# Kernel tuning notes

Measured on AMD Instinct MI355X. Metric: run time of the kernel, lower is better.

Reference implementation:

```python
import jax, jax.numpy as jnp
import numpy as np

BLOCK = 16
H = 16
KV = 4
HPG = H // KV
DH = 64
SCALE = 1.0 / np.sqrt(DH).astype(np.float32)


def setup_inputs() -> dict:
    key = jax.random.key(0)
    ks = jax.random.split(key, 7)
    B, Ldec, Lenc, D = 2, 8192, 4096, 1024
    s = 1.0 / np.sqrt(D).astype(np.float32)
    return {
        "hidden_states": jax.random.normal(ks[0], (B, Ldec, D), jnp.float32),
        "encoder_hidden_states": jax.random.normal(ks[1], (B, Lenc, D), jnp.float32),
        "attention_mask": jax.random.randint(ks[2], (B, Lenc), 0, 2, jnp.int32),
        "Wq": jax.random.normal(ks[3], (D, H * DH), jnp.float32) * s,
        "Wk": jax.random.normal(ks[4], (D, KV * DH), jnp.float32) * s,
        "Wv": jax.random.normal(ks[5], (D, KV * DH), jnp.float32) * s,
        "Wo": jax.random.normal(ks[6], (H * DH, D), jnp.float32) * s,
    }


def reference(hidden_states, encoder_hidden_states, attention_mask, Wq, Wk, Wv, Wo):
    B, Ldec, D = hidden_states.shape
    Lenc = encoder_hidden_states.shape[1]
    pad = (BLOCK - Ldec % BLOCK) % BLOCK
    x = jnp.pad(hidden_states, ((0, 0), (0, pad), (0, 0))) if pad else hidden_states
    nb = (Ldec + pad) // BLOCK
    # mean-pool decoder tokens into blocks: [B, nb, D]
    pooled = x.reshape(B, nb, BLOCK, D).mean(axis=2)
    # projections; GQA: group q heads by kv head (repeat_interleave order)
    q = (pooled @ Wq).reshape(B, nb, KV, HPG, DH)          # [B, nb, KV, HPG, DH]
    k = (encoder_hidden_states @ Wk).reshape(B, Lenc, KV, DH)
    v = (encoder_hidden_states @ Wv).reshape(B, Lenc, KV, DH)
    scores = jnp.einsum("bngqd,blgd->bgqnl", q, k) * SCALE  # [B, KV, HPG, nb, Lenc]
    mask = (attention_mask == 0)[:, None, None, None, :]
    scores = jnp.where(mask, jnp.float32(-1e9), scores)
    attn = jax.nn.softmax(scores, axis=-1)
    out = jnp.einsum("bgqnl,blgd->bngqd", attn, v)          # [B, nb, KV, HPG, DH]
    out = out.reshape(B, nb, H * DH) @ Wo                   # [B, nb, D]
    # broadcast block output back to token level
    unpooled = jnp.broadcast_to(out[:, :, None, :], (B, nb, BLOCK, D)).reshape(B, nb * BLOCK, D)
    return unpooled[:, :Ldec, :]
```

## Files before the change

kernel.cpp:

```cpp
#include <hip/hip_runtime.h>


typedef unsigned short u16;
typedef __attribute__((ext_vector_type(8))) __bf16 bf16x8;
typedef __attribute__((ext_vector_type(4))) float f32x4;
typedef __attribute__((ext_vector_type(4))) _Float16 f16x4;

static __device__ __forceinline__ u16 f2bf(float f) {
    unsigned int u = __float_as_uint(f);
    u = (u + 0x7fffu + ((u >> 16) & 1u)) >> 16;
    return (u16)u;
}
static __device__ __forceinline__ void gload16(const u16* g, u16* l) {
    __builtin_amdgcn_global_load_lds(
        (const __attribute__((address_space(1))) void*)g,
        (__attribute__((address_space(3))) void*)l, 16, 0, 0);
}

__global__ __launch_bounds__(256) void prep_all(const float* __restrict__ enc,
                                                const float* __restrict__ hid,
                                                const int* __restrict__ mask,
                                                const float* __restrict__ Wq,
                                                const float* __restrict__ Wk,
                                                const float* __restrict__ Wv,
                                                const float* __restrict__ Wo,
                                                u16* __restrict__ encb,
                                                u16* __restrict__ poolb,
                                                u16* __restrict__ mh,
                                                u16* __restrict__ Wq_t,
                                                u16* __restrict__ Wkv_t,
                                                u16* __restrict__ Wo_t) {
    int bid = blockIdx.x;
    if (bid < 1024) {
        const int tid = bid * 256 + threadIdx.x;
        const int c4 = tid & 255;
        const int row = tid >> 8;
        const float4* src = (const float4*)(hid + (size_t)row * 16 * 1024) + c4;
        float4 a = src[0];
#pragma unroll
        for (int t = 1; t < 16; ++t) {
            float4 b = src[(size_t)t * 256];
            a.x += b.x; a.y += b.y; a.z += b.z; a.w += b.w;
        }
        ushort4 o;
        o.x = f2bf(a.x * 0.0625f); o.y = f2bf(a.y * 0.0625f);
        o.z = f2bf(a.z * 0.0625f); o.w = f2bf(a.w * 0.0625f);
        *(ushort4*)(poolb + (size_t)row * 1024 + c4 * 4) = o;
    } else if (bid < 3072) {
        const int base = (bid - 1024) * 1024 + threadIdx.x;
        float4 v[4];
#pragma unroll
        for (int j = 0; j < 4; ++j) v[j] = ((const float4*)enc)[base + j * 256];
#pragma unroll
        for (int j = 0; j < 4; ++j) {
            ushort4 o;
            o.x = f2bf(v[j].x); o.y = f2bf(v[j].y);
            o.z = f2bf(v[j].z); o.w = f2bf(v[j].w);
            ((ushort4*)encb)[base + j * 256] = o;
        }
    } else if (bid < 5632) {
        bid -= 3072;
        const float* in; u16* out; int N, nbx, rowoff;
        if (bid < 1024)      { in = Wq; out = Wq_t;  N = 1024; nbx = 32; rowoff = 0; }
        else if (bid < 2048) { in = Wo; out = Wo_t;  N = 1024; nbx = 32; rowoff = 0; bid -= 1024; }
        else if (bid < 2304) { in = Wk; out = Wkv_t; N = 256;  nbx = 8;  rowoff = 0; bid -= 2048; }
        else                 { in = Wv; out = Wkv_t; N = 256;  nbx = 8;  rowoff = 256; bid -= 2304; }
        const int n0 = (bid % nbx) * 32, k0 = (bid / nbx) * 32;
        __shared__ float t[32][33];
        const int tx = threadIdx.x & 31, ty = threadIdx.x >> 5;
#pragma unroll
        for (int i = 0; i < 4; ++i)
            t[ty + 8 * i][tx] = in[(size_t)(k0 + ty + 8 * i) * N + n0 + tx];
        __syncthreads();
#pragma unroll
        for (int i = 0; i < 4; ++i)
            out[(size_t)(rowoff + n0 + ty + 8 * i) * 1024 + k0 + tx] = f2bf(t[tx][ty + 8 * i]);
    } else {
#pragma unroll
        for (int k = 0; k < 32; ++k) {
            const int i = threadIdx.x + 256 * k;
            mh[i] = mask[i] ? (u16)0x3C00 : (u16)0;
        }
    }
}

template <int MODE>
static __device__ __forceinline__ void gemm_core(const u16* __restrict__ A,
                                                 const u16* __restrict__ Bt,
                                                 u16* __restrict__ outQ,
                                                 float* __restrict__ out_f,
                                                 int m0, int n0, int kt0, int nkt,
                                                 u16* sAB) {
    u16* sA = sAB;
    u16* sB = sAB + 64 * 64;
    const int t = threadIdx.x;
    const int w = t >> 6, lane = t & 63, quad = lane >> 4, r16 = lane & 15;
    const int row8 = lane >> 3, seg = lane & 7;

    f32x4 acc[4];
#pragma unroll
    for (int i = 0; i < 4; ++i) acc[i] = (f32x4){0.f, 0.f, 0.f, 0.f};

    for (int kt = kt0; kt < kt0 + nkt; ++kt) {
        const int k0 = kt * 64;
        __syncthreads();
#pragma unroll
        for (int j = 0; j < 2; ++j) {
            const int ra = w * 16 + j * 8;
            gload16(A + (size_t)(m0 + ra + row8) * 1024 + k0 + seg * 8, sA + ra * 64);
            gload16(Bt + (size_t)(n0 + ra + row8) * 1024 + k0 + seg * 8, sB + ra * 64);
        }
        __syncthreads();
#pragma unroll
        for (int kk = 0; kk < 2; ++kk) {
            const bf16x8 af = *(const bf16x8*)(sA + (16 * w + r16) * 64 + kk * 32 + quad * 8);
#pragma unroll
            for (int nt = 0; nt < 4; ++nt) {
                const bf16x8 bfv = *(const bf16x8*)(sB + (nt * 16 + r16) * 64 + kk * 32 + quad * 8);
                acc[nt] = __builtin_amdgcn_mfma_f32_16x16x32_bf16(af, bfv, acc[nt], 0, 0, 0);
            }
        }
    }

    if (MODE == 0) {
#pragma unroll
        for (int nt = 0; nt < 4; ++nt)
#pragma unroll
            for (int r = 0; r < 4; ++r) {
                const int m = m0 + 16 * w + quad * 4 + r;
                const int c = n0 + nt * 16 + r16;
                const int b = m >> 9, nq = m & 511, g = c >> 8, qh = (c >> 6) & 3, d = c & 63;
                outQ[((((size_t)(b * 4 + g) * 4 + qh) * 512 + nq) << 6) + d] =
                    f2bf(acc[nt][r] * 0.180336880f);
            }
    } else {
#pragma unroll
        for (int nt = 0; nt < 4; ++nt)
#pragma unroll
            for (int r = 0; r < 4; ++r) {
                const int m = m0 + 16 * w + quad * 4 + r;
                const int c = n0 + nt * 16 + r16;
                out_f[(size_t)m * 1024 + c] = acc[nt][r];
            }
    }
}

__global__ __launch_bounds__(256) void gemm_qkv(const u16* __restrict__ poolb,
                                                const u16* __restrict__ encb,
                                                const u16* __restrict__ Wq_t,
                                                const u16* __restrict__ Wkv_t,
                                                const int* __restrict__ maskp,
                                                u16* __restrict__ Qa,
                                                u16* __restrict__ Ka,
                                                u16* __restrict__ Va) {
    __shared__ __align__(16) u16 smem[12288];
    const int bx = blockIdx.x;
    if (bx >= 512) {
        const int b = bx - 512;
        gemm_core<0>(poolb, Wq_t, Qa, nullptr, (b >> 4) * 64, (b & 15) * 64, 0, 16, smem);
        return;
    }
    const int m0 = (bx >> 3) * 128, n0 = (bx & 7) * 64;
    u16* sA = smem;
    u16* sB = smem + 128 * 64;
    const int t = threadIdx.x;
    const int w = t >> 6, lane = t & 63, quad = lane >> 4, r16 = lane & 15;
    const int row8 = lane >> 3, seg = lane & 7;

    f32x4 acc[2][4];
#pragma unroll
    for (int i = 0; i < 2; ++i)
#pragma unroll
        for (int nt = 0; nt < 4; ++nt) acc[i][nt] = (f32x4){0.f, 0.f, 0.f, 0.f};

    for (int kt = 0; kt < 16; ++kt) {
        const int k0 = kt * 64;
        __syncthreads();
#pragma unroll
        for (int p = 0; p < 4; ++p) {
            const int ra = p * 32 + w * 8;
            gload16(encb + (size_t)(m0 + ra + row8) * 1024 + k0 + seg * 8, sA + ra * 64);
        }
#pragma unroll
        for (int p = 0; p < 2; ++p) {
            const int ra = p * 32 + w * 8;
            gload16(Wkv_t + (size_t)(n0 + ra + row8) * 1024 + k0 + seg * 8, sB + ra * 64);
        }
        __syncthreads();
#pragma unroll
        for (int kk = 0; kk < 2; ++kk)
#pragma unroll
            for (int i = 0; i < 2; ++i) {
                const bf16x8 af = *(const bf16x8*)(sA + (w * 32 + i * 16 + r16) * 64 + kk * 32 + quad * 8);
#pragma unroll
                for (int nt = 0; nt < 4; ++nt) {
                    const bf16x8 bfv = *(const bf16x8*)(sB + (nt * 16 + r16) * 64 + kk * 32 + quad * 8);
                    acc[i][nt] = __builtin_amdgcn_mfma_f32_16x16x32_bf16(af, bfv, acc[i][nt], 0, 0, 0);
                }
            }
    }

    const bool isV = (n0 >= 256);
    const int g = (isV ? (n0 - 256) : n0) >> 6;
    const int b = m0 >> 12, l0 = m0 & 4095;
    __syncthreads();
    if (isV) {
        u16* sT = smem;
#pragma unroll
        for (int i = 0; i < 2; ++i) {
            float mfl[4];
#pragma unroll
            for (int r = 0; r < 4; ++r)
                mfl[r] = maskp[b * 4096 + l0 + w * 32 + i * 16 + quad * 4 + r] ? 1.f : 0.f;
#pragma unroll
            for (int nt = 0; nt < 4; ++nt)
#pragma unroll
                for (int r = 0; r < 4; ++r) {
                    const int ml = w * 32 + i * 16 + quad * 4 + r, cl = nt * 16 + r16;
                    union { _Float16 h; u16 u; } cv;
                    cv.h = (_Float16)(acc[i][nt][r] * mfl[r]);
                    sT[cl * 136 + ml] = cv.u;
                }
        }
        __syncthreads();
#pragma unroll
        for (int p = 0; p < 4; ++p) {
            const int idx = t + 256 * p, rr = idx >> 4, ch = idx & 15;
            *(int4*)(Va + ((size_t)(b * 4 + g) * 64 + rr) * 4096 + l0 + ch * 8) =
                *(const int4*)(sT + rr * 136 + ch * 8);
        }
    } else {
        u16* sT = smem;
#pragma unroll
        for (int i = 0; i < 2; ++i)
#pragma unroll
            for (int nt = 0; nt < 4; ++nt)
#pragma unroll
                for (int r = 0; r < 4; ++r) {
                    const int ml = w * 32 + i * 16 + quad * 4 + r, cl = nt * 16 + r16;
                    sT[ml * 72 + cl] = f2bf(acc[i][nt][r]);
                }
        __syncthreads();
#pragma unroll
        for (int p = 0; p < 4; ++p) {
            const int idx = t + 256 * p, rr = idx >> 3, ch = idx & 7;
            *(int4*)(Ka + (((size_t)(b * 4 + g) * 4096 + l0 + rr) << 6) + ch * 8) =
                *(const int4*)(sT + rr * 72 + ch * 8);
        }
    }
}

__global__ __launch_bounds__(256) void gemm_o(const u16* __restrict__ attn,
                                              const u16* __restrict__ Wo_t,
                                              float* __restrict__ blkpart) {
    __shared__ __align__(16) u16 smem[8192];
    const int bx = blockIdx.x;
    const int s = bx >> 8, m0 = ((bx >> 4) & 15) * 64, n0 = (bx & 15) * 64;
    gemm_core<3>(attn, Wo_t, nullptr, blkpart + ((size_t)s << 20), m0, n0, s * 4, 4, smem);
}

__global__ __launch_bounds__(256, 4) void flash_attn(const u16* __restrict__ Qa,
                                                     const u16* __restrict__ Ka,
                                                     const u16* __restrict__ Vt,
                                                     const u16* __restrict__ mh,
                                                     float* __restrict__ Opart,
                                                     float* __restrict__ mlpart) {
    const int bx = blockIdx.x;
    const int s16 = bx & 31, rr = bx >> 5;
    const int split = rr & 3, gb = rr >> 2;
    const int g = gb & 3, b = gb >> 2;
    __shared__ __align__(16) u16 sK[64 * 72];
    __shared__ __align__(16) u16 sV[64 * 68];
    const int t = threadIdx.x;
    const int qh = t >> 6, lane = t & 63, quad = lane >> 4, r16 = lane & 15;

    bf16x8 aq[2];
    {
        const size_t qbase = ((((size_t)(b * 4 + g) * 4 + qh) * 512) + s16 * 16 + r16) * 64;
#pragma unroll
        for (int kk = 0; kk < 2; ++kk)
            aq[kk] = *(const bf16x8*)(Qa + qbase + kk * 32 + quad * 8);
    }
    const u16* Kg = Ka + (size_t)(b * 4 + g) * 4096 * 64 + (size_t)split * 1024 * 64;
    const u16* Vg = Vt + (size_t)(b * 4 + g) * 64 * 4096 + split * 1024;
    const u16* mb = mh + b * 4096 + split * 1024 + quad * 4;

    f32x4 o[4], lacc;
#pragma unroll
    for (int i = 0; i < 4; ++i) o[i] = (f32x4){0.f, 0.f, 0.f, 0.f};
    lacc = (f32x4){0.f, 0.f, 0.f, 0.f};

    for (int tile = 0; tile < 16; ++tile) {
        const int l0 = tile * 64;
        __syncthreads();
#pragma unroll
        for (int p = 0; p < 2; ++p) {
            const int idx = t + 256 * p, row = idx >> 3, seg = idx & 7;
            *(int4*)(sK + row * 72 + seg * 8) =
                *(const int4*)(Kg + (size_t)(l0 + row) * 64 + seg * 8);
            *(int4*)(sV + row * 68 + seg * 8) =
                *(const int4*)(Vg + (size_t)row * 4096 + l0 + seg * 8);
        }
        __syncthreads();

        f32x4 st[4];
#pragma unroll
        for (int nt = 0; nt < 4; ++nt) st[nt] = (f32x4){0.f, 0.f, 0.f, 0.f};
#pragma unroll
        for (int kk = 0; kk < 2; ++kk)
#pragma unroll
            for (int nt = 0; nt < 4; ++nt) {
                const bf16x8 ka = *(const bf16x8*)(sK + (nt * 16 + r16) * 72 + kk * 32 + quad * 8);
                st[nt] = __builtin_amdgcn_mfma_f32_16x16x32_bf16(ka, aq[kk], st[nt], 0, 0, 0);
            }

#pragma unroll
        for (int nt = 0; nt < 4; ++nt) {
            f16x4 pa;
#pragma unroll
            for (int j = 0; j < 4; ++j)
                pa[j] = (_Float16)__builtin_amdgcn_exp2f(st[nt][j]);
            const f16x4 bvm = *(const f16x4*)(mb + l0 + nt * 16);
            lacc = __builtin_amdgcn_mfma_f32_16x16x16f16(pa, bvm, lacc, 0, 0, 0);
#pragma unroll
            for (int dt = 0; dt < 4; ++dt) {
                const f16x4 bv = *(const f16x4*)(sV + (dt * 16 + r16) * 68 + nt * 16 + quad * 4);
                o[dt] = __builtin_amdgcn_mfma_f32_16x16x16f16(pa, bv, o[dt], 0, 0, 0);
            }
        }
    }

    const size_t pbase = ((size_t)bx * 4 + qh) * 1024;
#pragma unroll
    for (int dt = 0; dt < 4; ++dt)
#pragma unroll
        for (int r = 0; r < 4; ++r)
            Opart[pbase + (size_t)(quad * 4 + r) * 64 + dt * 16 + r16] = o[dt][r];
    if (r16 == 0) {
#pragma unroll
        for (int r = 0; r < 4; ++r)
            mlpart[((size_t)bx * 4 + qh) * 16 + quad * 4 + r] = lacc[r];
    }
}

__global__ __launch_bounds__(256) void flash_combine(const float* __restrict__ Opart,
                                                     const float* __restrict__ mlpart,
                                                     u16* __restrict__ attnout) {
    const int bx = blockIdx.x;
    const int s16 = bx & 31, h = bx >> 5;
    const int qh = h & 3, g = (h >> 2) & 3, b = h >> 4;
    const int t = threadIdx.x;
    const int q = t >> 4, dg = t & 15;
    float4 a = make_float4(0.f, 0.f, 0.f, 0.f);
    float L = 0.f;
#pragma unroll
    for (int s = 0; s < 4; ++s) {
        const size_t part = (((size_t)((b * 4 + g) * 4 + s) * 32 + s16) * 4 + qh);
        const float4 v = *(const float4*)(Opart + part * 1024 + q * 64 + dg * 4);
        a.x += v.x; a.y += v.y; a.z += v.z; a.w += v.w;
        L += mlpart[part * 16 + q];
    }
    const float invL = 1.f / L;
    ushort4 ov;
    ov.x = f2bf(a.x * invL); ov.y = f2bf(a.y * invL);
    ov.z = f2bf(a.z * invL); ov.w = f2bf(a.w * invL);
    *(ushort4*)(attnout + ((size_t)b * 512 + s16 * 16 + q) * 1024 +
                (g * 4 + qh) * 64 + dg * 4) = ov;
}

__global__ __launch_bounds__(256) void bcast_out(const float* __restrict__ blkpart,
                                                 float* __restrict__ out) {
    const int tid = blockIdx.x * 256 + threadIdx.x;
    const int c4 = tid & 255;
    const int row = tid >> 8;
    float4 a = make_float4(0.f, 0.f, 0.f, 0.f);
#pragma unroll
    for (int s = 0; s < 4; ++s) {
        const float4 v = ((const float4*)blkpart)[(s << 18) + (row << 8) + c4];
        a.x += v.x; a.y += v.y; a.z += v.z; a.w += v.w;
    }
    const int b = row >> 9, n = row & 511;
    float4* dst = (float4*)out + (((size_t)b * 8192 + n * 16) << 8) + c4;
#pragma unroll
    for (int rep = 0; rep < 16; ++rep)
        dst[(size_t)rep << 8] = a;
}

extern "C" void kernel_launch(void* const* d_in, const int* in_sizes, int n_in,
                              void* d_out, int out_size, void* d_ws, size_t ws_size,
                              hipStream_t stream) {
    const float* hid  = (const float*)d_in[0];
    const float* enc  = (const float*)d_in[1];
    const int*   mask = (const int*)d_in[2];
    const float* Wq   = (const float*)d_in[3];
    const float* Wk   = (const float*)d_in[4];
    const float* Wv   = (const float*)d_in[5];
    const float* Wo   = (const float*)d_in[6];
    float* out = (float*)d_out;

    char* ws = (char*)d_ws;
    size_t off = 0;
    auto alloc = [&](size_t bytes) -> char* {
        char* p = ws + off;
        off += (bytes + 255) & ~(size_t)255;
        return p;
    };
    u16* Wq_t  = (u16*)alloc((size_t)1024 * 1024 * 2);
    u16* Wkv_t = (u16*)alloc((size_t)512 * 1024 * 2);
    u16* Wo_t  = (u16*)alloc((size_t)1024 * 1024 * 2);
    u16* encb  = (u16*)alloc((size_t)8192 * 1024 * 2);
    u16* poolb = (u16*)alloc((size_t)1024 * 1024 * 2);
    u16* Qa    = (u16*)alloc((size_t)1024 * 1024 * 2);
    u16* Ka    = (u16*)alloc((size_t)8 * 4096 * 64 * 2);
    u16* Va    = (u16*)alloc((size_t)8 * 4096 * 64 * 2);
    u16* attn  = (u16*)alloc((size_t)1024 * 1024 * 2);
    u16* mh    = (u16*)alloc((size_t)8192 * 2);
    float* Opart   = (float*)encb;
    float* blkpart = (float*)encb;
    float* mlpart  = (float*)poolb;

    prep_all<<<5633, 256, 0, stream>>>(enc, hid, mask, Wq, Wk, Wv, Wo,
                                       encb, poolb, mh, Wq_t, Wkv_t, Wo_t);
    gemm_qkv<<<768, 256, 0, stream>>>(poolb, encb, Wq_t, Wkv_t, mask, Qa, Ka, Va);
    flash_attn<<<1024, 256, 0, stream>>>(Qa, Ka, Va, mh, Opart, mlpart);
    flash_combine<<<1024, 256, 0, stream>>>(Opart, mlpart, attn);
    gemm_o<<<1024, 256, 0, stream>>>(attn, Wo_t, blkpart);
    bcast_out<<<1024, 256, 0, stream>>>(blkpart, out);
}
```

Before: 241.2 us.

## Fuse output projection with token broadcast and widen prep loads

Replaces the split-K output GEMM plus separate broadcast kernel with one kernel. It computes each 64x64 output tile over the full K, using double-buffered LDS staging via global_load_lds, and writes the 16-way broadcast to the output directly. This removes the fp32 partial buffer round trip and one launch. In exchange the grid drops from 1024 to 256 blocks with a longer serial K loop. The prep kernel also loads all 16 pooled rows up front with a tree reduction, and converts 8 float4 per thread for the encoder cast, which reduces block count.

```diff
diff --git a/kernel.cpp b/kernel.cpp
--- a/kernel.cpp
+++ b/kernel.cpp
@@ -32,34 +32,46 @@
                                                 u16* __restrict__ Wo_t) {
     int bid = blockIdx.x;
     if (bid < 1024) {
-        const int tid = bid * 256 + threadIdx.x;
-        const int c4 = tid & 255;
-        const int row = tid >> 8;
+        const int row = bid;
+        const int c4 = threadIdx.x;
         const float4* src = (const float4*)(hid + (size_t)row * 16 * 1024) + c4;
-        float4 a = src[0];
-#pragma unroll
-        for (int t = 1; t < 16; ++t) {
-            float4 b = src[(size_t)t * 256];
-            a.x += b.x; a.y += b.y; a.z += b.z; a.w += b.w;
-        }
+        float4 v[16];
+#pragma unroll
+        for (int t = 0; t < 16; ++t) v[t] = src[(size_t)t * 256];
+#pragma unroll
+        for (int t = 0; t < 8; ++t) {
+            v[t].x += v[t + 8].x; v[t].y += v[t + 8].y;
+            v[t].z += v[t + 8].z; v[t].w += v[t + 8].w;
+        }
+#pragma unroll
+        for (int t = 0; t < 4; ++t) {
+            v[t].x += v[t + 4].x; v[t].y += v[t + 4].y;
+            v[t].z += v[t + 4].z; v[t].w += v[t + 4].w;
+        }
+#pragma unroll
+        for (int t = 0; t < 2; ++t) {
+            v[t].x += v[t + 2].x; v[t].y += v[t + 2].y;
+            v[t].z += v[t + 2].z; v[t].w += v[t + 2].w;
+        }
+        v[0].x += v[1].x; v[0].y += v[1].y; v[0].z += v[1].z; v[0].w += v[1].w;
         ushort4 o;
-        o.x = f2bf(a.x * 0.0625f); o.y = f2bf(a.y * 0.0625f);
-        o.z = f2bf(a.z * 0.0625f); o.w = f2bf(a.w * 0.0625f);
+        o.x = f2bf(v[0].x * 0.0625f); o.y = f2bf(v[0].y * 0.0625f);
+        o.z = f2bf(v[0].z * 0.0625f); o.w = f2bf(v[0].w * 0.0625f);
         *(ushort4*)(poolb + (size_t)row * 1024 + c4 * 4) = o;
-    } else if (bid < 3072) {
-        const int base = (bid - 1024) * 1024 + threadIdx.x;
-        float4 v[4];
-#pragma unroll
-        for (int j = 0; j < 4; ++j) v[j] = ((const float4*)enc)[base + j * 256];
-#pragma unroll
-        for (int j = 0; j < 4; ++j) {
+    } else if (bid < 2048) {
+        const int base = (bid - 1024) * 2048 + threadIdx.x;
+        float4 v[8];
+#pragma unroll
+        for (int j = 0; j < 8; ++j) v[j] = ((const float4*)enc)[base + j * 256];
+#pragma unroll
+        for (int j = 0; j < 8; ++j) {
             ushort4 o;
             o.x = f2bf(v[j].x); o.y = f2bf(v[j].y);
             o.z = f2bf(v[j].z); o.w = f2bf(v[j].w);
             ((ushort4*)encb)[base + j * 256] = o;
         }
-    } else if (bid < 5632) {
-        bid -= 3072;
+    } else if (bid < 4608) {
+        bid -= 2048;
         const float* in; u16* out; int N, nbx, rowoff;
         if (bid < 1024)      { in = Wq; out = Wq_t;  N = 1024; nbx = 32; rowoff = 0; }
         else if (bid < 2048) { in = Wo; out = Wo_t;  N = 1024; nbx = 32; rowoff = 0; bid -= 1024; }
@@ -250,13 +262,67 @@
     }
 }
 
-__global__ __launch_bounds__(256) void gemm_o(const u16* __restrict__ attn,
-                                              const u16* __restrict__ Wo_t,
-                                              float* __restrict__ blkpart) {
-    __shared__ __align__(16) u16 smem[8192];
+__global__ __launch_bounds__(256) void gemm_o_bcast(const u16* __restrict__ attn,
+                                                    const u16* __restrict__ Wo_t,
+                                                    float* __restrict__ out) {
+    __shared__ __align__(16) u16 smem[2][8192];
+    __shared__ __align__(16) float sf[64 * 68];
     const int bx = blockIdx.x;
-    const int s = bx >> 8, m0 = ((bx >> 4) & 15) * 64, n0 = (bx & 15) * 64;
-    gemm_core<3>(attn, Wo_t, nullptr, blkpart + ((size_t)s << 20), m0, n0, s * 4, 4, smem);
+    const int m0 = (bx >> 4) * 64, n0 = (bx & 15) * 64;
+    const int t = threadIdx.x;
+    const int w = t >> 6, lane = t & 63, quad = lane >> 4, r16 = lane & 15;
+    const int row8 = lane >> 3, seg = lane & 7;
+
+    f32x4 acc[4];
+#pragma unroll
+    for (int i = 0; i < 4; ++i) acc[i] = (f32x4){0.f, 0.f, 0.f, 0.f};
+
+    auto stage = [&](int kt, int bi) {
+        const int k0 = kt * 64;
+        u16* sA = smem[bi];
+        u16* sB = smem[bi] + 4096;
+#pragma unroll
+        for (int j = 0; j < 2; ++j) {
+            const int ra = w * 16 + j * 8;
+            gload16(attn + (size_t)(m0 + ra + row8) * 1024 + k0 + seg * 8, sA + ra * 64);
+            gload16(Wo_t + (size_t)(n0 + ra + row8) * 1024 + k0 + seg * 8, sB + ra * 64);
+        }
+    };
+    stage(0, 0);
+    for (int kt = 0; kt < 16; ++kt) {
+        const int bi = kt & 1;
+        __syncthreads();
+        if (kt < 15) stage(kt + 1, bi ^ 1);
+        const u16* sA = smem[bi];
+        const u16* sB = smem[bi] + 4096;
+#pragma unroll
+        for (int kk = 0; kk < 2; ++kk) {
+            const bf16x8 af = *(const bf16x8*)(sA + (16 * w + r16) * 64 + kk * 32 + quad * 8);
+#pragma unroll
+            for (int nt = 0; nt < 4; ++nt) {
+                const bf16x8 bfv = *(const bf16x8*)(sB + (nt * 16 + r16) * 64 + kk * 32 + quad * 8);
+                acc[nt] = __builtin_amdgcn_mfma_f32_16x16x32_bf16(af, bfv, acc[nt], 0, 0, 0);
+            }
+        }
+    }
+    __syncthreads();
+#pragma unroll
+    for (int nt = 0; nt < 4; ++nt)
+#pragma unroll
+        for (int r = 0; r < 4; ++r)
+            sf[(16 * w + quad * 4 + r) * 68 + nt * 16 + r16] = acc[nt][r];
+    __syncthreads();
+    const int rr = t >> 4, ch = t & 15;
+#pragma unroll
+    for (int i = 0; i < 4; ++i) {
+        const int row = i * 16 + rr;
+        const int m = m0 + row, b = m >> 9, n = m & 511;
+        const float4 v = *(const float4*)(sf + row * 68 + ch * 4);
+        float4* dst = (float4*)(out + ((size_t)b * 8192 + (size_t)n * 16) * 1024 + n0) + ch;
+#pragma unroll
+        for (int rep = 0; rep < 16; ++rep)
+            dst[(size_t)rep * 256] = v;
+    }
 }
 
 __global__ __launch_bounds__(256, 4) void flash_attn(const u16* __restrict__ Qa,
@@ -366,24 +432,6 @@
     ov.z = f2bf(a.z * invL); ov.w = f2bf(a.w * invL);
     *(ushort4*)(attnout + ((size_t)b * 512 + s16 * 16 + q) * 1024 +
                 (g * 4 + qh) * 64 + dg * 4) = ov;
-}
-
-__global__ __launch_bounds__(256) void bcast_out(const float* __restrict__ blkpart,
-                                                 float* __restrict__ out) {
-    const int tid = blockIdx.x * 256 + threadIdx.x;
-    const int c4 = tid & 255;
-    const int row = tid >> 8;
-    float4 a = make_float4(0.f, 0.f, 0.f, 0.f);
-#pragma unroll
-    for (int s = 0; s < 4; ++s) {
-        const float4 v = ((const float4*)blkpart)[(s << 18) + (row << 8) + c4];
-        a.x += v.x; a.y += v.y; a.z += v.z; a.w += v.w;
-    }
-    const int b = row >> 9, n = row & 511;
-    float4* dst = (float4*)out + (((size_t)b * 8192 + n * 16) << 8) + c4;
-#pragma unroll
-    for (int rep = 0; rep < 16; ++rep)
-        dst[(size_t)rep << 8] = a;
 }
 
 extern "C" void kernel_launch(void* const* d_in, const int* in_sizes, int n_in,
@@ -415,15 +463,13 @@
     u16* Va    = (u16*)alloc((size_t)8 * 4096 * 64 * 2);
     u16* attn  = (u16*)alloc((size_t)1024 * 1024 * 2);
     u16* mh    = (u16*)alloc((size_t)8192 * 2);
-    float* Opart   = (float*)encb;
-    float* blkpart = (float*)encb;
-    float* mlpart  = (float*)poolb;
-
-    prep_all<<<5633, 256, 0, stream>>>(enc, hid, mask, Wq, Wk, Wv, Wo,
+    float* Opart  = (float*)encb;
+    float* mlpart = (float*)poolb;
+
+    prep_all<<<4609, 256, 0, stream>>>(enc, hid, mask, Wq, Wk, Wv, Wo,
                                        encb, poolb, mh, Wq_t, Wkv_t, Wo_t);
     gemm_qkv<<<768, 256, 0, stream>>>(poolb, encb, Wq_t, Wkv_t, mask, Qa, Ka, Va);
     flash_attn<<<1024, 256, 0, stream>>>(Qa, Ka, Va, mh, Opart, mlpart);
     flash_combine<<<1024, 256, 0, stream>>>(Opart, mlpart, attn);
-    gemm_o<<<1024, 256, 0, stream>>>(attn, Wo_t, blkpart);
-    bcast_out<<<1024, 256, 0, stream>>>(blkpart, out);
-}
+    gemm_o_bcast<<<256, 256, 0, stream>>>(attn, Wo_t, out);
+}
```

Result: no change. 240.8 us (-0.2%).
